# Optimization experiments

Measured on AMD Instinct MI355X. Metric: run time of the kernel, lower is better.

The kernel has to match this reference:

```python
import jax, jax.numpy as jnp
import numpy as np

CLASS_NUM = 6
N = 8388608


def setup_inputs() -> dict:
    key = jax.random.key(0)
    k1, k2, k3 = jax.random.split(key, 3)
    inputs = jax.random.normal(k1, (N, CLASS_NUM), dtype=jnp.float32)
    targets = jax.random.randint(k2, (N, 1), 0, CLASS_NUM, dtype=jnp.int32)
    # learned parameter: torch.rand(class_num) -> uniform [0,1)
    class_weight = jax.random.uniform(k3, (CLASS_NUM,), dtype=jnp.float32)
    return {"inputs": inputs, "targets": targets, "class_weight": class_weight}


def reference(inputs, targets, class_weight):
    # weighted argmax over classes: [N]
    preds = jnp.argmax(class_weight * inputs, axis=-1)
    tgt = targets.reshape(-1)  # [N]
    # confusion_matrix[pred, target] += 1  (data-dependent scatter-add histogram)
    cm = jnp.zeros((CLASS_NUM, CLASS_NUM), dtype=jnp.float32)
    cm = cm.at[preds, tgt].add(1.0)
    precision = jnp.diag(cm) / cm.sum(axis=0)
    recall = jnp.diag(cm) / cm.sum(axis=1)
    f1 = 2.0 * precision * recall / (precision + recall)
    loss = -f1.mean()
    return (loss, class_weight)
```

## Files before the change

### kernel.cpp

```cpp
#include <hip/hip_runtime.h>

#define CLS 6

constexpr int HIST_BLOCKS  = 2048;
constexpr int HIST_THREADS = 256;
constexpr int NCOPY        = 4;
constexpr int CM_STRIDE    = 40;

__global__ __launch_bounds__(HIST_THREADS, 8)
void cm_hist_kernel(const float* __restrict__ inputs,
                    const int*   __restrict__ targets,
                    const float* __restrict__ wts,
                    unsigned int* __restrict__ cm,
                    long long n_rows) {
    __shared__ unsigned int cm_s[NCOPY * CM_STRIDE];
    const int tid = threadIdx.x;
    if (tid < NCOPY * CM_STRIDE) cm_s[tid] = 0u;
    __syncthreads();

    const float w0 = wts[0], w1 = wts[1], w2 = wts[2];
    const float w3 = wts[3], w4 = wts[4], w5 = wts[5];

    const float4* __restrict__ in4 = (const float4*)inputs;
    const int2*   __restrict__ tg2 = (const int2*)targets;

    const int copy_base = (tid & (NCOPY - 1)) * CM_STRIDE;

    const long long n_pairs = n_rows >> 1;
    const long long stride  = (long long)gridDim.x * blockDim.x;

    for (long long p = (long long)blockIdx.x * blockDim.x + tid;
         p < n_pairs; p += stride) {
        float4 a = in4[3 * p + 0];
        float4 b = in4[3 * p + 1];
        float4 c = in4[3 * p + 2];
        int2   t = tg2[p];

        {
            float v0 = a.x * w0, v1 = a.y * w1, v2 = a.z * w2;
            float v3 = a.w * w3, v4 = b.x * w4, v5 = b.y * w5;
            int   pr = 0; float m = v0;
            if (v1 > m) { m = v1; pr = 1; }
            if (v2 > m) { m = v2; pr = 2; }
            if (v3 > m) { m = v3; pr = 3; }
            if (v4 > m) { m = v4; pr = 4; }
            if (v5 > m) { m = v5; pr = 5; }
            atomicAdd(&cm_s[copy_base + pr * CLS + t.x], 1u);
        }
        {
            float v0 = b.z * w0, v1 = b.w * w1, v2 = c.x * w2;
            float v3 = c.y * w3, v4 = c.z * w4, v5 = c.w * w5;
            int   pr = 0; float m = v0;
            if (v1 > m) { m = v1; pr = 1; }
            if (v2 > m) { m = v2; pr = 2; }
            if (v3 > m) { m = v3; pr = 3; }
            if (v4 > m) { m = v4; pr = 4; }
            if (v5 > m) { m = v5; pr = 5; }
            atomicAdd(&cm_s[copy_base + pr * CLS + t.y], 1u);
        }
    }

    if (blockIdx.x == 0 && tid == 0 && (n_rows & 1)) {
        long long r = n_rows - 1;
        int   pr = 0;
        float m  = inputs[r * CLS + 0] * w0;
        float v;
        v = inputs[r * CLS + 1] * w1; if (v > m) { m = v; pr = 1; }
        v = inputs[r * CLS + 2] * w2; if (v > m) { m = v; pr = 2; }
        v = inputs[r * CLS + 3] * w3; if (v > m) { m = v; pr = 3; }
        v = inputs[r * CLS + 4] * w4; if (v > m) { m = v; pr = 4; }
        v = inputs[r * CLS + 5] * w5; if (v > m) { m = v; pr = 5; }
        atomicAdd(&cm_s[pr * CLS + targets[r]], 1u);
    }

    __syncthreads();
    if (tid < CLS * CLS) {
        unsigned int v = cm_s[tid]
                       + cm_s[CM_STRIDE + tid]
                       + cm_s[2 * CM_STRIDE + tid]
                       + cm_s[3 * CM_STRIDE + tid];
        atomicAdd(&cm[tid], v);
    }
}

__global__ void macro_score_kernel(const unsigned int* __restrict__ cm,
                                   const float* __restrict__ wts,
                                   float* __restrict__ out) {
    if (threadIdx.x == 0) {
        float c[CLS * CLS];
        #pragma unroll
        for (int i = 0; i < CLS * CLS; ++i) c[i] = (float)cm[i];
        float f1sum = 0.0f;
        #pragma unroll
        for (int i = 0; i < CLS; ++i) {
            float col = 0.0f, row = 0.0f;
            #pragma unroll
            for (int j = 0; j < CLS; ++j) {
                col += c[j * CLS + i];
                row += c[i * CLS + j];
            }
            float d  = c[i * CLS + i];
            float pr = d / col;
            float rc = d / row;
            f1sum += 2.0f * pr * rc / (pr + rc);
        }
        out[0] = -(f1sum / (float)CLS);
    }
    if (threadIdx.x < CLS) out[1 + threadIdx.x] = wts[threadIdx.x];
}

extern "C" void kernel_launch(void* const* d_in, const int* in_sizes, int n_in,
                              void* d_out, int out_size, void* d_ws, size_t ws_size,
                              hipStream_t stream) {
    const float* inputs  = (const float*)d_in[0];
    const int*   targets = (const int*)d_in[1];
    const float* wts     = (const float*)d_in[2];
    float*       out     = (float*)d_out;
    unsigned int* cm     = (unsigned int*)d_ws;

    const long long n_rows = (long long)in_sizes[0] / CLS;

    hipMemsetAsync(cm, 0, CLS * CLS * sizeof(unsigned int), stream);
    cm_hist_kernel<<<HIST_BLOCKS, HIST_THREADS, 0, stream>>>(inputs, targets, wts, cm, n_rows);
    macro_score_kernel<<<1, 64, 0, stream>>>(cm, wts, out);
}
```

Before: 303.6 us.

## Fuse score kernel via last-block ticket and process four rows per thread

```diff
diff --git a/kernel.cpp b/kernel.cpp
--- a/kernel.cpp
+++ b/kernel.cpp
@@ -7,13 +7,27 @@
 constexpr int NCOPY        = 4;
 constexpr int CM_STRIDE    = 40;
 
-__global__ __launch_bounds__(HIST_THREADS, 8)
-void cm_hist_kernel(const float* __restrict__ inputs,
-                    const int*   __restrict__ targets,
-                    const float* __restrict__ wts,
-                    unsigned int* __restrict__ cm,
-                    long long n_rows) {
+__device__ __forceinline__ int argmax6(float v0, float v1, float v2,
+                                       float v3, float v4, float v5) {
+    int   pr = 0; float m = v0;
+    if (v1 > m) { m = v1; pr = 1; }
+    if (v2 > m) { m = v2; pr = 2; }
+    if (v3 > m) { m = v3; pr = 3; }
+    if (v4 > m) { m = v4; pr = 4; }
+    if (v5 > m) { m = v5; pr = 5; }
+    return pr;
+}
+
+__global__ __launch_bounds__(HIST_THREADS)
+void macro_fused_kernel(const float* __restrict__ inputs,
+                        const int*   __restrict__ targets,
+                        const float* __restrict__ wts,
+                        unsigned int* __restrict__ cm,
+                        unsigned int* __restrict__ ticket,
+                        float* __restrict__ out,
+                        long long n_rows) {
     __shared__ unsigned int cm_s[NCOPY * CM_STRIDE];
+    __shared__ bool is_last;
     const int tid = threadIdx.x;
     if (tid < NCOPY * CM_STRIDE) cm_s[tid] = 0u;
     __syncthreads();
@@ -22,55 +36,42 @@
     const float w3 = wts[3], w4 = wts[4], w5 = wts[5];
 
     const float4* __restrict__ in4 = (const float4*)inputs;
-    const int2*   __restrict__ tg2 = (const int2*)targets;
+    const int4*   __restrict__ tg4 = (const int4*)targets;
 
     const int copy_base = (tid & (NCOPY - 1)) * CM_STRIDE;
 
-    const long long n_pairs = n_rows >> 1;
+    const long long n_quads = n_rows >> 2;
     const long long stride  = (long long)gridDim.x * blockDim.x;
 
-    for (long long p = (long long)blockIdx.x * blockDim.x + tid;
-         p < n_pairs; p += stride) {
-        float4 a = in4[3 * p + 0];
-        float4 b = in4[3 * p + 1];
-        float4 c = in4[3 * p + 2];
-        int2   t = tg2[p];
+    for (long long q = (long long)blockIdx.x * blockDim.x + tid;
+         q < n_quads; q += stride) {
+        const long long b = 6 * q;
+        float4 f0 = in4[b + 0];
+        float4 f1 = in4[b + 1];
+        float4 f2 = in4[b + 2];
+        float4 f3 = in4[b + 3];
+        float4 f4 = in4[b + 4];
+        float4 f5 = in4[b + 5];
+        int4   t  = tg4[q];
 
-        {
-            float v0 = a.x * w0, v1 = a.y * w1, v2 = a.z * w2;
-            float v3 = a.w * w3, v4 = b.x * w4, v5 = b.y * w5;
-            int   pr = 0; float m = v0;
-            if (v1 > m) { m = v1; pr = 1; }
-            if (v2 > m) { m = v2; pr = 2; }
-            if (v3 > m) { m = v3; pr = 3; }
-            if (v4 > m) { m = v4; pr = 4; }
-            if (v5 > m) { m = v5; pr = 5; }
-            atomicAdd(&cm_s[copy_base + pr * CLS + t.x], 1u);
-        }
-        {
-            float v0 = b.z * w0, v1 = b.w * w1, v2 = c.x * w2;
-            float v3 = c.y * w3, v4 = c.z * w4, v5 = c.w * w5;
-            int   pr = 0; float m = v0;
-            if (v1 > m) { m = v1; pr = 1; }
-            if (v2 > m) { m = v2; pr = 2; }
-            if (v3 > m) { m = v3; pr = 3; }
-            if (v4 > m) { m = v4; pr = 4; }
-            if (v5 > m) { m = v5; pr = 5; }
-            atomicAdd(&cm_s[copy_base + pr * CLS + t.y], 1u);
-        }
+        int p0 = argmax6(f0.x * w0, f0.y * w1, f0.z * w2, f0.w * w3, f1.x * w4, f1.y * w5);
+        int p1 = argmax6(f1.z * w0, f1.w * w1, f2.x * w2, f2.y * w3, f2.z * w4, f2.w * w5);
+        int p2 = argmax6(f3.x * w0, f3.y * w1, f3.z * w2, f3.w * w3, f4.x * w4, f4.y * w5);
+        int p3 = argmax6(f4.z * w0, f4.w * w1, f5.x * w2, f5.y * w3, f5.z * w4, f5.w * w5);
+
+        atomicAdd(&cm_s[copy_base + p0 * CLS + t.x], 1u);
+        atomicAdd(&cm_s[copy_base + p1 * CLS + t.y], 1u);
+        atomicAdd(&cm_s[copy_base + p2 * CLS + t.z], 1u);
+        atomicAdd(&cm_s[copy_base + p3 * CLS + t.w], 1u);
     }
 
-    if (blockIdx.x == 0 && tid == 0 && (n_rows & 1)) {
-        long long r = n_rows - 1;
-        int   pr = 0;
-        float m  = inputs[r * CLS + 0] * w0;
-        float v;
-        v = inputs[r * CLS + 1] * w1; if (v > m) { m = v; pr = 1; }
-        v = inputs[r * CLS + 2] * w2; if (v > m) { m = v; pr = 2; }
-        v = inputs[r * CLS + 3] * w3; if (v > m) { m = v; pr = 3; }
-        v = inputs[r * CLS + 4] * w4; if (v > m) { m = v; pr = 4; }
-        v = inputs[r * CLS + 5] * w5; if (v > m) { m = v; pr = 5; }
-        atomicAdd(&cm_s[pr * CLS + targets[r]], 1u);
+    if (blockIdx.x == 0 && tid == 0) {
+        for (long long r = (n_quads << 2); r < n_rows; ++r) {
+            int pr = argmax6(inputs[r * CLS + 0] * w0, inputs[r * CLS + 1] * w1,
+                             inputs[r * CLS + 2] * w2, inputs[r * CLS + 3] * w3,
+                             inputs[r * CLS + 4] * w4, inputs[r * CLS + 5] * w5);
+            atomicAdd(&cm_s[pr * CLS + targets[r]], 1u);
+        }
     }
 
     __syncthreads();
@@ -79,34 +80,43 @@
                        + cm_s[CM_STRIDE + tid]
                        + cm_s[2 * CM_STRIDE + tid]
                        + cm_s[3 * CM_STRIDE + tid];
-        atomicAdd(&cm[tid], v);
+        if (v) atomicAdd(&cm[tid], v);
     }
-}
 
-__global__ void macro_score_kernel(const unsigned int* __restrict__ cm,
-                                   const float* __restrict__ wts,
-                                   float* __restrict__ out) {
-    if (threadIdx.x == 0) {
-        float c[CLS * CLS];
-        #pragma unroll
-        for (int i = 0; i < CLS * CLS; ++i) c[i] = (float)cm[i];
-        float f1sum = 0.0f;
-        #pragma unroll
-        for (int i = 0; i < CLS; ++i) {
-            float col = 0.0f, row = 0.0f;
+    if (blockIdx.x == 0 && tid < CLS) out[1 + tid] = wts[tid];
+
+    __syncthreads();
+    if (tid == 0) {
+        __threadfence();
+        unsigned int prev = atomicAdd(ticket, 1u);
+        is_last = (prev == (unsigned int)(gridDim.x - 1));
+    }
+    __syncthreads();
+
+    if (is_last) {
+        if (tid < CLS * CLS) cm_s[tid] = atomicAdd(&cm[tid], 0u);
+        __syncthreads();
+        if (tid == 0) {
+            float c[CLS * CLS];
             #pragma unroll
-            for (int j = 0; j < CLS; ++j) {
-                col += c[j * CLS + i];
-                row += c[i * CLS + j];
+            for (int i = 0; i < CLS * CLS; ++i) c[i] = (float)cm_s[i];
+            float f1sum = 0.0f;
+            #pragma unroll
+            for (int i = 0; i < CLS; ++i) {
+                float col = 0.0f, row = 0.0f;
+                #pragma unroll
+                for (int j = 0; j < CLS; ++j) {
+                    col += c[j * CLS + i];
+                    row += c[i * CLS + j];
+                }
+                float d  = c[i * CLS + i];
+                float pr = d / col;
+                float rc = d / row;
+                f1sum += 2.0f * pr * rc / (pr + rc);
             }
-            float d  = c[i * CLS + i];
-            float pr = d / col;
-            float rc = d / row;
-            f1sum += 2.0f * pr * rc / (pr + rc);
+            out[0] = -(f1sum / (float)CLS);
         }
-        out[0] = -(f1sum / (float)CLS);
     }
-    if (threadIdx.x < CLS) out[1 + threadIdx.x] = wts[threadIdx.x];
 }
 
 extern "C" void kernel_launch(void* const* d_in, const int* in_sizes, int n_in,
@@ -117,10 +127,11 @@
     const float* wts     = (const float*)d_in[2];
     float*       out     = (float*)d_out;
     unsigned int* cm     = (unsigned int*)d_ws;
+    unsigned int* ticket = cm + CLS * CLS;
 
     const long long n_rows = (long long)in_sizes[0] / CLS;
 
-    hipMemsetAsync(cm, 0, CLS * CLS * sizeof(unsigned int), stream);
-    cm_hist_kernel<<<HIST_BLOCKS, HIST_THREADS, 0, stream>>>(inputs, targets, wts, cm, n_rows);
-    macro_score_kernel<<<1, 64, 0, stream>>>(cm, wts, out);
+    hipMemsetAsync(d_ws, 0, (CLS * CLS + 1) * sizeof(unsigned int), stream);
+    macro_fused_kernel<<<HIST_BLOCKS, HIST_THREADS, 0, stream>>>(
+        inputs, targets, wts, cm, ticket, out, n_rows);
 }
```

Result: slower. 398.6 us (+31.3%).
